# Kernel optimization log

Hardware: AMD Instinct MI355X
Metric: run time of the kernel (lower is better)

The kernel has to match this reference:

```python
import jax, jax.numpy as jnp
import numpy as np

HEADS = 12
HEAD_SIZE = 64
INF = 1e12  # K.infinity() in bert4keras

B, L, D = 8, 1024, 768


def setup_inputs() -> dict:
    key = jax.random.key(0)
    k1, k2 = jax.random.split(key)
    x = jax.random.normal(k1, (B, L, D), dtype=jnp.float32)
    W = jax.random.normal(k2, (D, HEADS * HEAD_SIZE * 2), dtype=jnp.float32) * (1.0 / np.sqrt(D))
    b = jnp.zeros((HEADS * HEAD_SIZE * 2,), dtype=jnp.float32)
    mask = jnp.ones((B, L), dtype=jnp.int32)
    return {"x": x, "W": W, "b": b, "mask": mask}


def _rope_sin_cos(seq_len, head_size, dtype):
    # SinusoidalPositionEmbedding(head_size, 'zero'):
    # emb[n, 2i] = sin(n * 10000^(-2i/S)), emb[n, 2i+1] = cos(...)
    pos = jnp.arange(seq_len, dtype=dtype)                       # [L]
    inv = jnp.power(jnp.asarray(10000.0, dtype),
                    -2.0 * jnp.arange(head_size // 2, dtype=dtype) / head_size)  # [S/2]
    ang = pos[:, None] * inv[None, :]                            # [L, S/2]
    # repeat_elements(..., 2, -1): [c0,c0,c1,c1,...]
    cos_pos = jnp.repeat(jnp.cos(ang), 2, axis=-1)               # [L, S]
    sin_pos = jnp.repeat(jnp.sin(ang), 2, axis=-1)               # [L, S]
    return sin_pos[None, :, None, :], cos_pos[None, :, None, :]  # [1,L,1,S]


def _rotate_half_interleaved(t):
    # stack([-t[...,1::2], t[...,::2]], -1).reshape(t.shape)
    t2 = jnp.stack([-t[..., 1::2], t[..., ::2]], axis=-1)
    return t2.reshape(t.shape)


def reference(x, W, b, mask):
    dtype = x.dtype
    Bq, Lq, _ = x.shape
    S = HEAD_SIZE
    # dense projection + head split: [B, L, H, 2S]
    proj = (jnp.einsum('bld,de->ble', x, W) + b).reshape(Bq, Lq, HEADS, 2 * S)
    qw, kw = proj[..., :S], proj[..., S:]
    # inline RoPE (interleaved variant)
    sin_pos, cos_pos = _rope_sin_cos(Lq, S, dtype)
    qw = qw * cos_pos + _rotate_half_interleaved(qw) * sin_pos
    kw = kw * cos_pos + _rotate_half_interleaved(kw) * sin_pos
    # bilinear score: [B, H, L, L]
    logits = jnp.einsum('bmhd,bnhd->bhmn', qw, kw)
    # padding mask on axis 2 (rows) and axis 3 (cols): x*m + (-INF)*(1-m)
    m = mask.astype(dtype)
    m_row = m[:, None, :, None]
    m_col = m[:, None, None, :]
    logits = logits * m_row + (-INF) * (1.0 - m_row)
    logits = logits * m_col + (-INF) * (1.0 - m_col)
    # upper-triangular (incl. diagonal) mask
    tri = jnp.triu(jnp.ones((Lq, Lq), dtype=dtype))
    logits = logits - (1.0 - tri) * INF
    return logits / np.sqrt(S).astype(np.float32)
```

## Files before the change

### kernel.cpp

```cpp
#include <hip/hip_runtime.h>
#include <hip/hip_bf16.h>
#include <stdint.h>

#define NHEADS 12
#define HS 64
#define NB 8
#define NL 1024
#define ND 768
#define NE 1536
#define INFV 1000000000000.0f

typedef __bf16 bf16x8 __attribute__((ext_vector_type(8)));
typedef float f32x4 __attribute__((ext_vector_type(4)));

typedef __attribute__((address_space(1))) const unsigned int gas_uint;
typedef __attribute__((address_space(3))) unsigned int las_uint;
#define GLOAD_LDS16(g, l) __builtin_amdgcn_global_load_lds((gas_uint*)(g), (las_uint*)(l), 16, 0, 0)

__device__ __forceinline__ unsigned short f2bf(float f) {
  unsigned int u = __builtin_bit_cast(unsigned int, f);
  u += 0x7fffu + ((u >> 16) & 1u);
  return (unsigned short)(u >> 16);
}

__device__ __forceinline__ bf16x8 load_frag(const unsigned short* p) {
  uint4 v = *(const uint4*)p;
  return __builtin_bit_cast(bf16x8, v);
}

__global__ __launch_bounds__(256) void k_prep(
    const float* __restrict__ x, const float* __restrict__ W,
    unsigned short* __restrict__ xb, unsigned short* __restrict__ wt,
    float* __restrict__ cst) {
  const int blk = blockIdx.x;
  if (blk < 6144) {
    int i = blk * 256 + threadIdx.x;
    float4 v = ((const float4*)x)[i];
    ushort4 o;
    o.x = f2bf(v.x); o.y = f2bf(v.y); o.z = f2bf(v.z); o.w = f2bf(v.w);
    ((ushort4*)xb)[i] = o;
  } else if (blk < 6144 + 288) {
    __shared__ float tile[64][65];
    int t = blk - 6144;
    int te = t % 24, td = t / 24;
    int c = threadIdx.x & 63, r4 = threadIdx.x >> 6;
    #pragma unroll
    for (int rr = 0; rr < 16; rr++) {
      int row = rr * 4 + r4;
      tile[row][c] = W[(size_t)(td * 64 + row) * NE + te * 64 + c];
    }
    __syncthreads();
    #pragma unroll
    for (int rr = 0; rr < 16; rr++) {
      int row = rr * 4 + r4;
      wt[(size_t)(te * 64 + row) * ND + td * 64 + c] = f2bf(tile[c][row]);
    }
  } else {
    int t = (blk - 6432) * 256 + threadIdx.x;
    int p = t >> 5, i = t & 31;
    float inv = powf(10000.0f, -(float)i / 32.0f);
    float sv, cv;
    sincosf((float)p * inv, &sv, &cv);
    cst[(p * 32 + i) * 2 + 0] = cv;
    cst[(p * 32 + i) * 2 + 1] = sv;
  }
}

__global__ __launch_bounds__(256, 4) void k_proj_fill(
    const unsigned short* __restrict__ xb,
    const unsigned short* __restrict__ wt,
    const float* __restrict__ bias,
    const float* __restrict__ cst,
    unsigned short* __restrict__ qbuf, unsigned short* __restrict__ kbuf,
    const int* __restrict__ mask, float* __restrict__ out) {
  const int tid = threadIdx.x;

  __shared__ char smem_b[32768];

  if (blockIdx.x >= 768) {
    const int e   = blockIdx.x - 768;
    const int bh  = e / 28;
    int u = e % 28;
    int tm = 1;
    #pragma unroll
    for (int k = 0; k < 6; k++) if (u >= tm) { u -= tm; tm++; }
    const int tn = u;
    const int b  = bh / NHEADS;
    const int* mrow = mask + b * NL;
    const int n0 = tn * 128 + (tid & 31) * 4;
    int4 mc = *(const int4*)&mrow[n0];
    float o0 = ((mc.x ? 0.0f : -INFV) - INFV) * 0.125f;
    float o1 = ((mc.y ? 0.0f : -INFV) - INFV) * 0.125f;
    float o2 = ((mc.z ? 0.0f : -INFV) - INFV) * 0.125f;
    float o3 = ((mc.w ? 0.0f : -INFV) - INFV) * 0.125f;
    const float oz = (-2.0f * INFV) * 0.125f;
    #pragma unroll
    for (int it = 0; it < 16; it++) {
      int m = tm * 128 + it * 8 + (tid >> 5);
      bool mr1 = (mrow[m] != 0);
      f32x4 o;
      o[0] = mr1 ? o0 : oz;
      o[1] = mr1 ? o1 : oz;
      o[2] = mr1 ? o2 : oz;
      o[3] = mr1 ? o3 : oz;
      __builtin_nontemporal_store(o, (f32x4*)(out + ((size_t)bh * NL + m) * NL + n0));
    }
    return;
  }

  const int blk = blockIdx.x;
  const int xcd = blk & 7;
  const int loc = blk >> 3;
  const int h   = loc % 12;
  const int mt  = xcd * 8 + loc / 12;
  const int m0  = mt * 128;
  const int e0  = h * 128;
  const int lane = tid & 63;
  const int w    = tid >> 6;
  const int wm = w >> 1, wn = w & 1;
  const int col_l = lane & 15, rq = lane >> 4;

  unsigned int goff[4];
  #pragma unroll
  for (int q = 0; q < 4; q++) {
    int p = q * 256 + tid;
    int r = p >> 3, sl = p & 7;
    goff[q] = r * ND + (sl ^ (r & 7)) * 8;
  }
  const unsigned short* gA = wt + (size_t)e0 * ND;
  const unsigned short* gB = xb + (size_t)m0 * ND;

  const int xr = col_l & 7;
  const unsigned int aRow = (unsigned)((wn * 64 + col_l) * 128);
  const unsigned int bRow = (unsigned)(16384 + (wm * 64 + col_l) * 128);

  f32x4 acc[4][4];
  #pragma unroll
  for (int i = 0; i < 4; i++)
    #pragma unroll
    for (int j = 0; j < 4; j++)
      #pragma unroll
      for (int q = 0; q < 4; q++) acc[i][j][q] = 0.0f;

  for (int kk = 0; kk < ND; kk += 64) {
    const unsigned short* sA = gA + kk;
    const unsigned short* sB = gB + kk;
    #pragma unroll
    for (int q = 0; q < 4; q++) GLOAD_LDS16(sA + goff[q], smem_b + (q * 256 + tid) * 16);
    #pragma unroll
    for (int q = 0; q < 4; q++) GLOAD_LDS16(sB + goff[q], smem_b + 16384 + (q * 256 + tid) * 16);
    __syncthreads();
    #pragma unroll
    for (int kkh = 0; kkh < 2; kkh++) {
      bf16x8 af[4], bfr[4];
      #pragma unroll
      for (int f = 0; f < 4; f++) {
        const unsigned int so = (((kkh << 2) | rq) ^ xr) * 16;
        af[f]  = __builtin_bit_cast(bf16x8, *(const uint4*)(smem_b + aRow + f * 2048 + so));
        bfr[f] = __builtin_bit_cast(bf16x8, *(const uint4*)(smem_b + bRow + f * 2048 + so));
      }
      #pragma unroll
      for (int i = 0; i < 4; i++)
        #pragma unroll
        for (int j = 0; j < 4; j++)
          acc[i][j] = __builtin_amdgcn_mfma_f32_16x16x32_bf16(af[i], bfr[j], acc[i][j], 0, 0, 0);
    }
    __syncthreads();
  }

  unsigned short* obuf = (wn == 1) ? kbuf : qbuf;
  #pragma unroll
  for (int j = 0; j < 4; j++) {
    const int m   = m0 + wm * 64 + j * 16 + col_l;
    const int pos = m & (NL - 1);
    const int bb  = m >> 10;
    const float* crow = cst + pos * 64;
    unsigned short* orow = obuf + (((size_t)(bb * NHEADS + h)) * NL + pos) * HS;
    #pragma unroll
    for (int i = 0; i < 4; i++) {
      const int s0 = i * 16 + rq * 4;
      float4 bv = *(const float4*)&bias[e0 + wn * 64 + s0];
      float4 tq = *(const float4*)(crow + s0);
      float v0 = acc[i][j][0] + bv.x;
      float v1 = acc[i][j][1] + bv.y;
      float v2 = acc[i][j][2] + bv.z;
      float v3 = acc[i][j][3] + bv.w;
      ushort4 o;
      o.x = f2bf(v0 * tq.x - v1 * tq.y);
      o.y = f2bf(v1 * tq.x + v0 * tq.y);
      o.z = f2bf(v2 * tq.z - v3 * tq.w);
      o.w = f2bf(v3 * tq.z + v2 * tq.w);
      *(ushort4*)&orow[s0] = o;
    }
  }
}

__global__ __launch_bounds__(256) void k_logits(
    const unsigned short* __restrict__ qbuf,
    const unsigned short* __restrict__ kbuf,
    const int* __restrict__ mask,
    float* __restrict__ out) {
  const int f  = blockIdx.x;
  const int r  = f & 7, t = f >> 3;
  const int bh = r + 8 * (t / 36);
  int u = t % 36;
  int tm = 0;
  #pragma unroll
  for (int k = 0; k < 7; k++) if (u >= 8 - tm) { u -= 8 - tm; tm++; }
  const int tn = tm + u;
  const int b  = bh / NHEADS;
  const int tid  = threadIdx.x;
  const int* mrow = mask + b * NL;

  const int lane = tid & 63;
  const int w    = tid >> 6;
  const int wm = w >> 1, wn = w & 1;
  const int m_base = tm * 128 + wm * 64;
  const int n_base = tn * 128 + wn * 64;
  const int col_l = lane & 15, rq = lane >> 4;
  const unsigned short* Q = qbuf + (size_t)bh * (NL * HS);
  const unsigned short* K = kbuf + (size_t)bh * (NL * HS);

  __shared__ float lds[64 * 132];

  f32x4 acc[4][4];
  #pragma unroll
  for (int i = 0; i < 4; i++)
    #pragma unroll
    for (int j = 0; j < 4; j++)
      #pragma unroll
      for (int q = 0; q < 4; q++) acc[i][j][q] = 0.0f;

  #pragma unroll
  for (int ks = 0; ks < 2; ks++) {
    bf16x8 ak[4], bq[4];
    #pragma unroll
    for (int ff = 0; ff < 4; ff++) {
      ak[ff] = load_frag(K + (size_t)(n_base + ff * 16 + col_l) * HS + ks * 32 + rq * 8);
      bq[ff] = load_frag(Q + (size_t)(m_base + ff * 16 + col_l) * HS + ks * 32 + rq * 8);
    }
    #pragma unroll
    for (int i = 0; i < 4; i++)
      #pragma unroll
      for (int j = 0; j < 4; j++)
        acc[i][j] = __builtin_amdgcn_mfma_f32_16x16x32_bf16(ak[i], bq[j], acc[i][j], 0, 0, 0);
  }

  const bool diag = (tn == tm);
  const int rb_row = tid >> 5;
  const int rb_c4  = (tid & 31) * 4;
  const int n_rb   = tn * 128 + rb_c4;
  int4 mc_rb = *(const int4*)&mrow[n_rb];
  const bool allmc = (mc_rb.x & mc_rb.y & mc_rb.z & mc_rb.w) != 0;

  #pragma unroll
  for (int pass = 0; pass < 2; pass++) {
    if (wm == pass) {
      #pragma unroll
      for (int j = 0; j < 4; j++) {
        const int rl = j * 16 + col_l;
        #pragma unroll
        for (int i = 0; i < 4; i++)
          *(f32x4*)&lds[rl * 132 + wn * 64 + i * 16 + rq * 4] = acc[i][j];
      }
    }
    __syncthreads();
    #pragma unroll
    for (int it = 0; it < 8; it++) {
      const int rl = it * 8 + rb_row;
      const int m  = tm * 128 + pass * 64 + rl;
      f32x4 v = *(const f32x4*)&lds[rl * 132 + rb_c4];
      if (mrow[m] == 0) { v[0] = -INFV; v[1] = -INFV; v[2] = -INFV; v[3] = -INFV; }
      if (!allmc) {
        if (mc_rb.x == 0) v[0] = -INFV;
        if (mc_rb.y == 0) v[1] = -INFV;
        if (mc_rb.z == 0) v[2] = -INFV;
        if (mc_rb.w == 0) v[3] = -INFV;
      }
      if (diag) {
        if (n_rb + 0 < m) v[0] -= INFV;
        if (n_rb + 1 < m) v[1] -= INFV;
        if (n_rb + 2 < m) v[2] -= INFV;
        if (n_rb + 3 < m) v[3] -= INFV;
      }
      v *= 0.125f;
      __builtin_nontemporal_store(v, (f32x4*)(out + ((size_t)bh * NL + m) * NL + n_rb));
    }
    __syncthreads();
  }
}

extern "C" void kernel_launch(void* const* d_in, const int* in_sizes, int n_in,
                              void* d_out, int out_size, void* d_ws, size_t ws_size,
                              hipStream_t stream) {
  const float* x    = (const float*)d_in[0];
  const float* W    = (const float*)d_in[1];
  const float* bias = (const float*)d_in[2];
  const int*   mask = (const int*)d_in[3];
  float* out = (float*)d_out;
  char* ws = (char*)d_ws;

  unsigned short* xb = (unsigned short*)(ws);
  unsigned short* wt = (unsigned short*)(ws + 12582912);
  unsigned short* qb = (unsigned short*)(ws + 14942208);
  unsigned short* kb = (unsigned short*)(ws + 27525120);
  float* cst = (float*)(ws + 40108032);

  k_prep<<<6560, 256, 0, stream>>>(x, W, xb, wt, cst);
  k_proj_fill<<<768 + 2688, 256, 0, stream>>>(xb, wt, bias, cst, qb, kb, mask, out);
  k_logits<<<3456, 256, 0, stream>>>(qb, kb, mask, out);
}
```

Measured before the change: 120.1 us.

## Merge projection and logits kernels into a cooperative persistent kernel with grid sync

Replaces the separate projection/fill and logits launches with one cooperative kernel of 1024 persistent blocks. Each block first does projection or strided fill tiles, then waits at a grid-wide barrier and loops over the logits tiles. The logits LDS staging buffer also moves from a padded row stride to an XOR-swizzled 128-float stride so it fits the shared 32KB buffer without bank conflicts. This is meant to cut launch overhead and the tail between kernels, at the cost of a grid barrier, less parallelism per phase, and a host-side occupancy query on every call, with a fallback to two plain launches.

Result: slower. 122.7 us (+2.2%).

```diff
diff --git a/kernel.cpp b/kernel.cpp
--- a/kernel.cpp
+++ b/kernel.cpp
@@ -1,6 +1,9 @@
 #include <hip/hip_runtime.h>
 #include <hip/hip_bf16.h>
+#include <hip/hip_cooperative_groups.h>
 #include <stdint.h>
+
+namespace cg = cooperative_groups;
 
 #define NHEADS 12
 #define HS 64
@@ -66,49 +69,41 @@
   }
 }
 
-__global__ __launch_bounds__(256, 4) void k_proj_fill(
-    const unsigned short* __restrict__ xb,
-    const unsigned short* __restrict__ wt,
-    const float* __restrict__ bias,
-    const float* __restrict__ cst,
-    unsigned short* __restrict__ qbuf, unsigned short* __restrict__ kbuf,
-    const int* __restrict__ mask, float* __restrict__ out) {
-  const int tid = threadIdx.x;
-
-  __shared__ char smem_b[32768];
-
-  if (blockIdx.x >= 768) {
-    const int e   = blockIdx.x - 768;
-    const int bh  = e / 28;
-    int u = e % 28;
-    int tm = 1;
-    #pragma unroll
-    for (int k = 0; k < 6; k++) if (u >= tm) { u -= tm; tm++; }
-    const int tn = u;
-    const int b  = bh / NHEADS;
-    const int* mrow = mask + b * NL;
-    const int n0 = tn * 128 + (tid & 31) * 4;
-    int4 mc = *(const int4*)&mrow[n0];
-    float o0 = ((mc.x ? 0.0f : -INFV) - INFV) * 0.125f;
-    float o1 = ((mc.y ? 0.0f : -INFV) - INFV) * 0.125f;
-    float o2 = ((mc.z ? 0.0f : -INFV) - INFV) * 0.125f;
-    float o3 = ((mc.w ? 0.0f : -INFV) - INFV) * 0.125f;
-    const float oz = (-2.0f * INFV) * 0.125f;
-    #pragma unroll
-    for (int it = 0; it < 16; it++) {
-      int m = tm * 128 + it * 8 + (tid >> 5);
-      bool mr1 = (mrow[m] != 0);
-      f32x4 o;
-      o[0] = mr1 ? o0 : oz;
-      o[1] = mr1 ? o1 : oz;
-      o[2] = mr1 ? o2 : oz;
-      o[3] = mr1 ? o3 : oz;
-      __builtin_nontemporal_store(o, (f32x4*)(out + ((size_t)bh * NL + m) * NL + n0));
-    }
-    return;
-  }
-
-  const int blk = blockIdx.x;
+__device__ __forceinline__ void dev_fill_tile(int e, const int* __restrict__ mask,
+                                              float* __restrict__ out, int tid) {
+  const int bh = e / 28;
+  int u = e % 28;
+  int tm = 1;
+  #pragma unroll
+  for (int kk = 0; kk < 6; kk++) if (u >= tm) { u -= tm; tm++; }
+  const int tn = u;
+  const int b  = bh / NHEADS;
+  const int* mrow = mask + b * NL;
+  const int n0 = tn * 128 + (tid & 31) * 4;
+  int4 mc = *(const int4*)&mrow[n0];
+  float o0 = ((mc.x ? 0.0f : -INFV) - INFV) * 0.125f;
+  float o1 = ((mc.y ? 0.0f : -INFV) - INFV) * 0.125f;
+  float o2 = ((mc.z ? 0.0f : -INFV) - INFV) * 0.125f;
+  float o3 = ((mc.w ? 0.0f : -INFV) - INFV) * 0.125f;
+  const float oz = (-2.0f * INFV) * 0.125f;
+  #pragma unroll
+  for (int it = 0; it < 16; it++) {
+    int m = tm * 128 + it * 8 + (tid >> 5);
+    bool mr1 = (mrow[m] != 0);
+    f32x4 o;
+    o[0] = mr1 ? o0 : oz;
+    o[1] = mr1 ? o1 : oz;
+    o[2] = mr1 ? o2 : oz;
+    o[3] = mr1 ? o3 : oz;
+    __builtin_nontemporal_store(o, (f32x4*)(out + ((size_t)bh * NL + m) * NL + n0));
+  }
+}
+
+__device__ __forceinline__ void dev_proj_tile(
+    int blk, int tid, char* smem_b,
+    const unsigned short* __restrict__ xb, const unsigned short* __restrict__ wt,
+    const float* __restrict__ bias, const float* __restrict__ cst,
+    unsigned short* __restrict__ qbuf, unsigned short* __restrict__ kbuf) {
   const int xcd = blk & 7;
   const int loc = blk >> 3;
   const int h   = loc % 12;
@@ -195,13 +190,11 @@
   }
 }
 
-__global__ __launch_bounds__(256) void k_logits(
-    const unsigned short* __restrict__ qbuf,
-    const unsigned short* __restrict__ kbuf,
-    const int* __restrict__ mask,
-    float* __restrict__ out) {
-  const int f  = blockIdx.x;
-  const int r  = f & 7, t = f >> 3;
+__device__ __forceinline__ void dev_logits_tile(
+    int t0, int tid, float* lds,
+    const unsigned short* __restrict__ qbuf, const unsigned short* __restrict__ kbuf,
+    const int* __restrict__ mask, float* __restrict__ out) {
+  const int r  = t0 & 7, t = t0 >> 3;
   const int bh = r + 8 * (t / 36);
   int u = t % 36;
   int tm = 0;
@@ -209,7 +202,6 @@
   for (int k = 0; k < 7; k++) if (u >= 8 - tm) { u -= 8 - tm; tm++; }
   const int tn = tm + u;
   const int b  = bh / NHEADS;
-  const int tid  = threadIdx.x;
   const int* mrow = mask + b * NL;
 
   const int lane = tid & 63;
@@ -221,8 +213,6 @@
   const unsigned short* Q = qbuf + (size_t)bh * (NL * HS);
   const unsigned short* K = kbuf + (size_t)bh * (NL * HS);
 
-  __shared__ float lds[64 * 132];
-
   f32x4 acc[4][4];
   #pragma unroll
   for (int i = 0; i < 4; i++)
@@ -259,9 +249,12 @@
       #pragma unroll
       for (int j = 0; j < 4; j++) {
         const int rl = j * 16 + col_l;
+        const int sw = (rl & 7) << 2;
         #pragma unroll
-        for (int i = 0; i < 4; i++)
-          *(f32x4*)&lds[rl * 132 + wn * 64 + i * 16 + rq * 4] = acc[i][j];
+        for (int i = 0; i < 4; i++) {
+          const int c = (wn * 64 + i * 16 + rq * 4) ^ sw;
+          *(f32x4*)&lds[rl * 128 + c] = acc[i][j];
+        }
       }
     }
     __syncthreads();
@@ -269,7 +262,8 @@
     for (int it = 0; it < 8; it++) {
       const int rl = it * 8 + rb_row;
       const int m  = tm * 128 + pass * 64 + rl;
-      f32x4 v = *(const f32x4*)&lds[rl * 132 + rb_c4];
+      const int c  = rb_c4 ^ ((rl & 7) << 2);
+      f32x4 v = *(const f32x4*)&lds[rl * 128 + c];
       if (mrow[m] == 0) { v[0] = -INFV; v[1] = -INFV; v[2] = -INFV; v[3] = -INFV; }
       if (!allmc) {
         if (mc_rb.x == 0) v[0] = -INFV;
@@ -290,6 +284,59 @@
   }
 }
 
+__global__ __launch_bounds__(256, 4) void k_mega(
+    const unsigned short* __restrict__ xb, const unsigned short* __restrict__ wt,
+    const float* __restrict__ bias, const float* __restrict__ cst,
+    unsigned short* __restrict__ qbuf, unsigned short* __restrict__ kbuf,
+    const int* __restrict__ mask, float* __restrict__ out) {
+  __shared__ char smem_b[32768];
+  const int tid = threadIdx.x;
+  const int blk = blockIdx.x;
+
+  if (blk >= 768) {
+    const int base = blk - 768;
+    #pragma unroll 1
+    for (int k = 0; k < 11; k++) {
+      const int e = base + 256 * k;
+      if (e >= 2688) break;
+      dev_fill_tile(e, mask, out, tid);
+    }
+  } else {
+    dev_proj_tile(blk, tid, smem_b, xb, wt, bias, cst, qbuf, kbuf);
+  }
+
+  __threadfence();
+  cg::this_grid().sync();
+
+  #pragma unroll 1
+  for (int kt = 0; kt < 4; kt++) {
+    const int t0 = blk + 1024 * kt;
+    if (t0 >= 3456) break;
+    dev_logits_tile(t0, tid, (float*)smem_b, qbuf, kbuf, mask, out);
+  }
+}
+
+__global__ __launch_bounds__(256, 4) void k_projfill(
+    const unsigned short* __restrict__ xb, const unsigned short* __restrict__ wt,
+    const float* __restrict__ bias, const float* __restrict__ cst,
+    unsigned short* __restrict__ qbuf, unsigned short* __restrict__ kbuf,
+    const int* __restrict__ mask, float* __restrict__ out) {
+  __shared__ char smem_b[32768];
+  const int tid = threadIdx.x;
+  if (blockIdx.x >= 768) {
+    dev_fill_tile(blockIdx.x - 768, mask, out, tid);
+    return;
+  }
+  dev_proj_tile(blockIdx.x, tid, smem_b, xb, wt, bias, cst, qbuf, kbuf);
+}
+
+__global__ __launch_bounds__(256) void k_logits_nc(
+    const unsigned short* __restrict__ qbuf, const unsigned short* __restrict__ kbuf,
+    const int* __restrict__ mask, float* __restrict__ out) {
+  __shared__ char smem_b[32768];
+  dev_logits_tile(blockIdx.x, threadIdx.x, (float*)smem_b, qbuf, kbuf, mask, out);
+}
+
 extern "C" void kernel_launch(void* const* d_in, const int* in_sizes, int n_in,
                               void* d_out, int out_size, void* d_ws, size_t ws_size,
                               hipStream_t stream) {
@@ -307,6 +354,25 @@
   float* cst = (float*)(ws + 40108032);
 
   k_prep<<<6560, 256, 0, stream>>>(x, W, xb, wt, cst);
-  k_proj_fill<<<768 + 2688, 256, 0, stream>>>(xb, wt, bias, cst, qb, kb, mask, out);
-  k_logits<<<3456, 256, 0, stream>>>(qb, kb, mask, out);
-}
+
+  int dev = 0, ncu = 0, occ = 0;
+  hipGetDevice(&dev);
+  hipDeviceGetAttribute(&ncu, hipDeviceAttributeMultiprocessorCount, dev);
+  hipOccupancyMaxActiveBlocksPerMultiprocessor(&occ, k_mega, 256, 0);
+
+  bool done = false;
+  if (occ >= 4 && (long)occ * ncu >= 1024) {
+    const unsigned short* xbc = xb;
+    const unsigned short* wtc = wt;
+    const float* cstc = cst;
+    void* args[8] = {(void*)&xbc, (void*)&wtc, (void*)&bias, (void*)&cstc,
+                     (void*)&qb, (void*)&kb, (void*)&mask, (void*)&out};
+    hipError_t err = hipLaunchCooperativeKernel(k_mega, dim3(1024), dim3(256),
+                                                args, 0, stream);
+    done = (err == hipSuccess);
+  }
+  if (!done) {
+    k_projfill<<<768 + 2688, 256, 0, stream>>>(xb, wt, bias, cst, qb, kb, mask, out);
+    k_logits_nc<<<3456, 256, 0, stream>>>(qb, kb, mask, out);
+  }
+}
```

## Pipeline projection and logits across batch slabs in a fused multi-launch kernel

Applied to the files above, without the earlier changes.

Merges the projection, logits and constant-fill work into one kernel, `k_pipe`, launched five times. Each launch projects Q/K for the next two batches while computing logits for the two batches projected in the previous launch, and it also writes a share of the masked fill tiles. The intent is to overlap the compute-heavy projection with the store-heavy logits and fill work and to remove the serial gap between the separate kernels. The logits LDS staging changes from a 132-float padded row to an XOR-swizzled 128-float row so it fits in the shared 32 KB buffer. The cost is extra launch overhead and partly filled tail waves in each of the five launches.

Measured after the change: 143.7 us. 19.6% more time.

```diff
diff --git a/kernel.cpp b/kernel.cpp
--- a/kernel.cpp
+++ b/kernel.cpp
@@ -66,53 +66,41 @@
   }
 }
 
-__global__ __launch_bounds__(256, 4) void k_proj_fill(
-    const unsigned short* __restrict__ xb,
-    const unsigned short* __restrict__ wt,
-    const float* __restrict__ bias,
-    const float* __restrict__ cst,
-    unsigned short* __restrict__ qbuf, unsigned short* __restrict__ kbuf,
-    const int* __restrict__ mask, float* __restrict__ out) {
-  const int tid = threadIdx.x;
-
-  __shared__ char smem_b[32768];
-
-  if (blockIdx.x >= 768) {
-    const int e   = blockIdx.x - 768;
-    const int bh  = e / 28;
-    int u = e % 28;
-    int tm = 1;
-    #pragma unroll
-    for (int k = 0; k < 6; k++) if (u >= tm) { u -= tm; tm++; }
-    const int tn = u;
-    const int b  = bh / NHEADS;
-    const int* mrow = mask + b * NL;
-    const int n0 = tn * 128 + (tid & 31) * 4;
-    int4 mc = *(const int4*)&mrow[n0];
-    float o0 = ((mc.x ? 0.0f : -INFV) - INFV) * 0.125f;
-    float o1 = ((mc.y ? 0.0f : -INFV) - INFV) * 0.125f;
-    float o2 = ((mc.z ? 0.0f : -INFV) - INFV) * 0.125f;
-    float o3 = ((mc.w ? 0.0f : -INFV) - INFV) * 0.125f;
-    const float oz = (-2.0f * INFV) * 0.125f;
-    #pragma unroll
-    for (int it = 0; it < 16; it++) {
-      int m = tm * 128 + it * 8 + (tid >> 5);
-      bool mr1 = (mrow[m] != 0);
-      f32x4 o;
-      o[0] = mr1 ? o0 : oz;
-      o[1] = mr1 ? o1 : oz;
-      o[2] = mr1 ? o2 : oz;
-      o[3] = mr1 ? o3 : oz;
-      __builtin_nontemporal_store(o, (f32x4*)(out + ((size_t)bh * NL + m) * NL + n0));
-    }
-    return;
-  }
-
-  const int blk = blockIdx.x;
-  const int xcd = blk & 7;
-  const int loc = blk >> 3;
-  const int h   = loc % 12;
-  const int mt  = xcd * 8 + loc / 12;
+__device__ __forceinline__ void dev_fill_tile(int e, const int* __restrict__ mask,
+                                              float* __restrict__ out, int tid) {
+  const int bh = e / 28;
+  int u = e % 28;
+  int tm = 1;
+  #pragma unroll
+  for (int kk = 0; kk < 6; kk++) if (u >= tm) { u -= tm; tm++; }
+  const int tn = u;
+  const int b  = bh / NHEADS;
+  const int* mrow = mask + b * NL;
+  const int n0 = tn * 128 + (tid & 31) * 4;
+  int4 mc = *(const int4*)&mrow[n0];
+  float o0 = ((mc.x ? 0.0f : -INFV) - INFV) * 0.125f;
+  float o1 = ((mc.y ? 0.0f : -INFV) - INFV) * 0.125f;
+  float o2 = ((mc.z ? 0.0f : -INFV) - INFV) * 0.125f;
+  float o3 = ((mc.w ? 0.0f : -INFV) - INFV) * 0.125f;
+  const float oz = (-2.0f * INFV) * 0.125f;
+  #pragma unroll
+  for (int it = 0; it < 16; it++) {
+    int m = tm * 128 + it * 8 + (tid >> 5);
+    bool mr1 = (mrow[m] != 0);
+    f32x4 o;
+    o[0] = mr1 ? o0 : oz;
+    o[1] = mr1 ? o1 : oz;
+    o[2] = mr1 ? o2 : oz;
+    o[3] = mr1 ? o3 : oz;
+    __builtin_nontemporal_store(o, (f32x4*)(out + ((size_t)bh * NL + m) * NL + n0));
+  }
+}
+
+__device__ __forceinline__ void dev_proj_tile(
+    int mt, int h, int tid, char* smem_b,
+    const unsigned short* __restrict__ xb, const unsigned short* __restrict__ wt,
+    const float* __restrict__ bias, const float* __restrict__ cst,
+    unsigned short* __restrict__ qbuf, unsigned short* __restrict__ kbuf) {
   const int m0  = mt * 128;
   const int e0  = h * 128;
   const int lane = tid & 63;
@@ -195,21 +183,15 @@
   }
 }
 
-__global__ __launch_bounds__(256) void k_logits(
-    const unsigned short* __restrict__ qbuf,
-    const unsigned short* __restrict__ kbuf,
-    const int* __restrict__ mask,
-    float* __restrict__ out) {
-  const int f  = blockIdx.x;
-  const int r  = f & 7, t = f >> 3;
-  const int bh = r + 8 * (t / 36);
-  int u = t % 36;
+__device__ __forceinline__ void dev_logits_tile(
+    int bh, int u, int tid, float* lds,
+    const unsigned short* __restrict__ qbuf, const unsigned short* __restrict__ kbuf,
+    const int* __restrict__ mask, float* __restrict__ out) {
   int tm = 0;
   #pragma unroll
   for (int k = 0; k < 7; k++) if (u >= 8 - tm) { u -= 8 - tm; tm++; }
   const int tn = tm + u;
   const int b  = bh / NHEADS;
-  const int tid  = threadIdx.x;
   const int* mrow = mask + b * NL;
 
   const int lane = tid & 63;
@@ -221,8 +203,6 @@
   const unsigned short* Q = qbuf + (size_t)bh * (NL * HS);
   const unsigned short* K = kbuf + (size_t)bh * (NL * HS);
 
-  __shared__ float lds[64 * 132];
-
   f32x4 acc[4][4];
   #pragma unroll
   for (int i = 0; i < 4; i++)
@@ -259,9 +239,12 @@
       #pragma unroll
       for (int j = 0; j < 4; j++) {
         const int rl = j * 16 + col_l;
+        const int sw = (rl & 7) << 2;
         #pragma unroll
-        for (int i = 0; i < 4; i++)
-          *(f32x4*)&lds[rl * 132 + wn * 64 + i * 16 + rq * 4] = acc[i][j];
+        for (int i = 0; i < 4; i++) {
+          const int c = (wn * 64 + i * 16 + rq * 4) ^ sw;
+          *(f32x4*)&lds[rl * 128 + c] = acc[i][j];
+        }
       }
     }
     __syncthreads();
@@ -269,7 +252,8 @@
     for (int it = 0; it < 8; it++) {
       const int rl = it * 8 + rb_row;
       const int m  = tm * 128 + pass * 64 + rl;
-      f32x4 v = *(const f32x4*)&lds[rl * 132 + rb_c4];
+      const int c  = rb_c4 ^ ((rl & 7) << 2);
+      f32x4 v = *(const f32x4*)&lds[rl * 128 + c];
       if (mrow[m] == 0) { v[0] = -INFV; v[1] = -INFV; v[2] = -INFV; v[3] = -INFV; }
       if (!allmc) {
         if (mc_rb.x == 0) v[0] = -INFV;
@@ -290,6 +274,32 @@
   }
 }
 
+__global__ __launch_bounds__(256, 4) void k_pipe(
+    const unsigned short* __restrict__ xb, const unsigned short* __restrict__ wt,
+    const float* __restrict__ bias, const float* __restrict__ cst,
+    unsigned short* __restrict__ qbuf, unsigned short* __restrict__ kbuf,
+    const int* __restrict__ mask, float* __restrict__ out,
+    int nproj, int mt_base, int nlog, int bh_base, int fill_base) {
+  __shared__ char smem_b[32768];
+  const int tid = threadIdx.x;
+  const int blk = blockIdx.x;
+
+  if (blk < nproj) {
+    const int xcd = blk & 7;
+    const int j   = blk >> 3;
+    const int mt  = mt_base + xcd * 2 + j / 12;
+    const int h   = j % 12;
+    dev_proj_tile(mt, h, tid, smem_b, xb, wt, bias, cst, qbuf, kbuf);
+  } else if (blk < nproj + nlog) {
+    const int i = blk - nproj;
+    const int r = i & 7, t = i >> 3;
+    const int bh = bh_base + r + 8 * (t / 36);
+    dev_logits_tile(bh, t % 36, tid, (float*)smem_b, qbuf, kbuf, mask, out);
+  } else {
+    dev_fill_tile(fill_base + (blk - nproj - nlog), mask, out, tid);
+  }
+}
+
 extern "C" void kernel_launch(void* const* d_in, const int* in_sizes, int n_in,
                               void* d_out, int out_size, void* d_ws, size_t ws_size,
                               hipStream_t stream) {
@@ -307,6 +317,15 @@
   float* cst = (float*)(ws + 40108032);
 
   k_prep<<<6560, 256, 0, stream>>>(x, W, xb, wt, cst);
-  k_proj_fill<<<768 + 2688, 256, 0, stream>>>(xb, wt, bias, cst, qb, kb, mask, out);
-  k_logits<<<3456, 256, 0, stream>>>(qb, kb, mask, out);
-}
+
+  k_pipe<<<192 + 0 + 538, 256, 0, stream>>>(xb, wt, bias, cst, qb, kb, mask, out,
+                                            192, 0, 0, 0, 0);
+  k_pipe<<<192 + 864 + 538, 256, 0, stream>>>(xb, wt, bias, cst, qb, kb, mask, out,
+                                              192, 16, 864, 0, 538);
+  k_pipe<<<192 + 864 + 538, 256, 0, stream>>>(xb, wt, bias, cst, qb, kb, mask, out,
+                                              192, 32, 864, 24, 1076);
+  k_pipe<<<192 + 864 + 538, 256, 0, stream>>>(xb, wt, bias, cst, qb, kb, mask, out,
+                                              192, 48, 864, 48, 1614);
+  k_pipe<<<0 + 864 + 536, 256, 0, stream>>>(xb, wt, bias, cst, qb, kb, mask, out,
+                                            0, 0, 864, 72, 2152);
+}
```

## Enlarge projection GEMM tile to 256x128 with 512 threads; swizzle logits LDS staging

Applied to the files above, without the earlier changes.

The projection GEMM now runs 512-thread blocks that each compute a 256-row by 128-column tile, halving the number of GEMM blocks. Each block reuses its weight tile across twice as many x rows, which cuts global and LDS traffic per output. Each wave holds 2x8 accumulators and loads A fragments once per k-step. The fill blocks now use 512 threads and do 8 iterations instead of 16. In the logits kernel, the padded LDS stride of 132 is replaced by stride 128 with an XOR swizzle to avoid bank conflicts while using less LDS. The larger block raises register and LDS pressure, and with only 384 GEMM blocks the GPU may be less evenly loaded.

Result: no change. 119.9 us (-0.2%).

```diff
diff --git a/kernel.cpp b/kernel.cpp
--- a/kernel.cpp
+++ b/kernel.cpp
@@ -66,28 +66,29 @@
   }
 }
 
-__global__ __launch_bounds__(256, 4) void k_proj_fill(
+__global__ __launch_bounds__(512, 4) void k_projfill(
     const unsigned short* __restrict__ xb,
     const unsigned short* __restrict__ wt,
     const float* __restrict__ bias,
     const float* __restrict__ cst,
     unsigned short* __restrict__ qbuf, unsigned short* __restrict__ kbuf,
     const int* __restrict__ mask, float* __restrict__ out) {
+  __shared__ char smem_b[49152];
   const int tid = threadIdx.x;
-
-  __shared__ char smem_b[32768];
-
-  if (blockIdx.x >= 768) {
-    const int e   = blockIdx.x - 768;
+  const int blk = blockIdx.x;
+
+  if (blk >= 384) {
+    const int e   = blk - 384;
     const int bh  = e / 28;
     int u = e % 28;
     int tm = 1;
     #pragma unroll
-    for (int k = 0; k < 6; k++) if (u >= tm) { u -= tm; tm++; }
+    for (int kk = 0; kk < 6; kk++) if (u >= tm) { u -= tm; tm++; }
     const int tn = u;
     const int b  = bh / NHEADS;
     const int* mrow = mask + b * NL;
     const int n0 = tn * 128 + (tid & 31) * 4;
+    const int row = tid >> 5;
     int4 mc = *(const int4*)&mrow[n0];
     float o0 = ((mc.x ? 0.0f : -INFV) - INFV) * 0.125f;
     float o1 = ((mc.y ? 0.0f : -INFV) - INFV) * 0.125f;
@@ -95,8 +96,8 @@
     float o3 = ((mc.w ? 0.0f : -INFV) - INFV) * 0.125f;
     const float oz = (-2.0f * INFV) * 0.125f;
     #pragma unroll
-    for (int it = 0; it < 16; it++) {
-      int m = tm * 128 + it * 8 + (tid >> 5);
+    for (int it = 0; it < 8; it++) {
+      int m = tm * 128 + it * 16 + row;
       bool mr1 = (mrow[m] != 0);
       f32x4 o;
       o[0] = mr1 ? o0 : oz;
@@ -108,37 +109,42 @@
     return;
   }
 
-  const int blk = blockIdx.x;
   const int xcd = blk & 7;
   const int loc = blk >> 3;
-  const int h   = loc % 12;
-  const int mt  = xcd * 8 + loc / 12;
-  const int m0  = mt * 128;
-  const int e0  = h * 128;
+  const int mt  = xcd * 4 + loc / 12;
+  const int et  = loc % 12;
+  const int m0  = mt * 256;
+  const int e0  = et * 128;
   const int lane = tid & 63;
   const int w    = tid >> 6;
-  const int wm = w >> 1, wn = w & 1;
+  const int wm = w >> 2, wn = w & 3;
   const int col_l = lane & 15, rq = lane >> 4;
 
-  unsigned int goff[4];
+  unsigned int goffA[2], goffB[4];
+  #pragma unroll
+  for (int q = 0; q < 2; q++) {
+    int p = q * 512 + tid;
+    int r = p >> 3, sl = p & 7;
+    goffA[q] = r * ND + (sl ^ (r & 7)) * 8;
+  }
   #pragma unroll
   for (int q = 0; q < 4; q++) {
-    int p = q * 256 + tid;
+    int p = q * 512 + tid;
     int r = p >> 3, sl = p & 7;
-    goff[q] = r * ND + (sl ^ (r & 7)) * 8;
+    goffB[q] = r * ND + (sl ^ (r & 7)) * 8;
   }
   const unsigned short* gA = wt + (size_t)e0 * ND;
   const unsigned short* gB = xb + (size_t)m0 * ND;
 
   const int xr = col_l & 7;
-  const unsigned int aRow = (unsigned)((wn * 64 + col_l) * 128);
-  const unsigned int bRow = (unsigned)(16384 + (wm * 64 + col_l) * 128);
-
-  f32x4 acc[4][4];
-  #pragma unroll
-  for (int i = 0; i < 4; i++)
-    #pragma unroll
-    for (int j = 0; j < 4; j++)
+  const unsigned int aRow = (unsigned)((wn * 32 + col_l) * 128);
+  const unsigned int bRow = (unsigned)(16384 + (wm * 128 + col_l) * 128);
+
+  f32x4 acc[2][8];
+  #pragma unroll
+  for (int i = 0; i < 2; i++)
+    #pragma unroll
+    for (int j = 0; j < 8; j++)
       #pragma unroll
       for (int q = 0; q < 4; q++) acc[i][j][q] = 0.0f;
 
@@ -146,40 +152,39 @@
     const unsigned short* sA = gA + kk;
     const unsigned short* sB = gB + kk;
     #pragma unroll
-    for (int q = 0; q < 4; q++) GLOAD_LDS16(sA + goff[q], smem_b + (q * 256 + tid) * 16);
-    #pragma unroll
-    for (int q = 0; q < 4; q++) GLOAD_LDS16(sB + goff[q], smem_b + 16384 + (q * 256 + tid) * 16);
+    for (int q = 0; q < 2; q++) GLOAD_LDS16(sA + goffA[q], smem_b + (q * 512 + tid) * 16);
+    #pragma unroll
+    for (int q = 0; q < 4; q++) GLOAD_LDS16(sB + goffB[q], smem_b + 16384 + (q * 512 + tid) * 16);
     __syncthreads();
     #pragma unroll
     for (int kkh = 0; kkh < 2; kkh++) {
-      bf16x8 af[4], bfr[4];
-      #pragma unroll
-      for (int f = 0; f < 4; f++) {
-        const unsigned int so = (((kkh << 2) | rq) ^ xr) * 16;
-        af[f]  = __builtin_bit_cast(bf16x8, *(const uint4*)(smem_b + aRow + f * 2048 + so));
-        bfr[f] = __builtin_bit_cast(bf16x8, *(const uint4*)(smem_b + bRow + f * 2048 + so));
+      const unsigned int so = (((kkh << 2) | rq) ^ xr) * 16;
+      bf16x8 af0 = __builtin_bit_cast(bf16x8, *(const uint4*)(smem_b + aRow + 0 * 2048 + so));
+      bf16x8 af1 = __builtin_bit_cast(bf16x8, *(const uint4*)(smem_b + aRow + 1 * 2048 + so));
+      #pragma unroll
+      for (int j = 0; j < 8; j++) {
+        bf16x8 bfr = __builtin_bit_cast(bf16x8, *(const uint4*)(smem_b + bRow + j * 2048 + so));
+        acc[0][j] = __builtin_amdgcn_mfma_f32_16x16x32_bf16(af0, bfr, acc[0][j], 0, 0, 0);
+        acc[1][j] = __builtin_amdgcn_mfma_f32_16x16x32_bf16(af1, bfr, acc[1][j], 0, 0, 0);
       }
-      #pragma unroll
-      for (int i = 0; i < 4; i++)
-        #pragma unroll
-        for (int j = 0; j < 4; j++)
-          acc[i][j] = __builtin_amdgcn_mfma_f32_16x16x32_bf16(af[i], bfr[j], acc[i][j], 0, 0, 0);
-    }
-    __syncthreads();
-  }
-
-  unsigned short* obuf = (wn == 1) ? kbuf : qbuf;
-  #pragma unroll
-  for (int j = 0; j < 4; j++) {
-    const int m   = m0 + wm * 64 + j * 16 + col_l;
+    }
+    __syncthreads();
+  }
+
+  const bool isk = (wn >= 2);
+  unsigned short* obuf = isk ? kbuf : qbuf;
+  #pragma unroll
+  for (int j = 0; j < 8; j++) {
+    const int m   = m0 + wm * 128 + j * 16 + col_l;
     const int pos = m & (NL - 1);
     const int bb  = m >> 10;
     const float* crow = cst + pos * 64;
-    unsigned short* orow = obuf + (((size_t)(bb * NHEADS + h)) * NL + pos) * HS;
-    #pragma unroll
-    for (int i = 0; i < 4; i++) {
-      const int s0 = i * 16 + rq * 4;
-      float4 bv = *(const float4*)&bias[e0 + wn * 64 + s0];
+    unsigned short* orow = obuf + (((size_t)(bb * NHEADS + et)) * NL + pos) * HS;
+    #pragma unroll
+    for (int i = 0; i < 2; i++) {
+      const int sl0 = wn * 32 + i * 16 + rq * 4;
+      const int s0  = sl0 & 63;
+      float4 bv = *(const float4*)&bias[e0 + sl0];
       float4 tq = *(const float4*)(crow + s0);
       float v0 = acc[i][j][0] + bv.x;
       float v1 = acc[i][j][1] + bv.y;
@@ -221,7 +226,7 @@
   const unsigned short* Q = qbuf + (size_t)bh * (NL * HS);
   const unsigned short* K = kbuf + (size_t)bh * (NL * HS);
 
-  __shared__ float lds[64 * 132];
+  __shared__ float lds[64 * 128];
 
   f32x4 acc[4][4];
   #pragma unroll
@@ -259,9 +264,12 @@
       #pragma unroll
       for (int j = 0; j < 4; j++) {
         const int rl = j * 16 + col_l;
+        const int sw = (rl & 7) << 2;
         #pragma unroll
-        for (int i = 0; i < 4; i++)
-          *(f32x4*)&lds[rl * 132 + wn * 64 + i * 16 + rq * 4] = acc[i][j];
+        for (int i = 0; i < 4; i++) {
+          const int c = (wn * 64 + i * 16 + rq * 4) ^ sw;
+          *(f32x4*)&lds[rl * 128 + c] = acc[i][j];
+        }
       }
     }
     __syncthreads();
@@ -269,7 +277,8 @@
     for (int it = 0; it < 8; it++) {
       const int rl = it * 8 + rb_row;
       const int m  = tm * 128 + pass * 64 + rl;
-      f32x4 v = *(const f32x4*)&lds[rl * 132 + rb_c4];
+      const int c  = rb_c4 ^ ((rl & 7) << 2);
+      f32x4 v = *(const f32x4*)&lds[rl * 128 + c];
       if (mrow[m] == 0) { v[0] = -INFV; v[1] = -INFV; v[2] = -INFV; v[3] = -INFV; }
       if (!allmc) {
         if (mc_rb.x == 0) v[0] = -INFV;
@@ -307,6 +316,6 @@
   float* cst = (float*)(ws + 40108032);
 
   k_prep<<<6560, 256, 0, stream>>>(x, W, xb, wt, cst);
-  k_proj_fill<<<768 + 2688, 256, 0, stream>>>(xb, wt, bias, cst, qb, kb, mask, out);
+  k_projfill<<<384 + 2688, 512, 0, stream>>>(xb, wt, bias, cst, qb, kb, mask, out);
   k_logits<<<3456, 256, 0, stream>>>(qb, kb, mask, out);
 }
```
